# Performance work log

Hardware: AMD Instinct MI355X
Metric: run time of the kernel (lower is better)

Reference implementation:

```python
import jax, jax.numpy as jnp
import numpy as np

N = 1_000_000      # neurons (scaled-up NEURON_COUNT)
E = 20_000_000     # synapses (scaled-up NEURON_COUNT * SYNAPSE_RATIO)
IN = 4096          # input_size
OUT = 4096         # output_size
STEPS = 3


def setup_inputs() -> dict:
    key = jax.random.key(0)
    k1, k2, k3, k4, k5 = jax.random.split(key, 5)
    x = jax.random.normal(k1, (IN,), jnp.float32)
    synapse_src = jax.random.randint(k2, (E,), 0, N)
    synapse_dst = jax.random.randint(k3, (E,), 0, N)
    synapse_weights = jax.random.normal(k4, (E,), jnp.float32)
    neuron_biases = jax.random.normal(k5, (N - IN,), jnp.float32)
    input_indices = jnp.arange(IN)              # first IN neurons are inputs
    output_indices = jnp.arange(N - OUT, N)     # last OUT neurons are outputs
    non_input_indices = jnp.arange(IN, N)       # complement of input_indices
    return {
        "x": x,
        "synapse_weights": synapse_weights,
        "neuron_biases": neuron_biases,
        "synapse_src": synapse_src,
        "synapse_dst": synapse_dst,
        "input_indices": input_indices,
        "output_indices": output_indices,
        "non_input_indices": non_input_indices,
    }


def reference(x, synapse_weights, neuron_biases, synapse_src, synapse_dst,
              input_indices, output_indices, non_input_indices):
    # out_mask[i] True => neuron i is an output (skipped by tanh)
    out_mask = jnp.zeros(N, dtype=bool).at[output_indices].set(True)
    # initial state: zeros with inputs written in
    v = jnp.zeros(N, dtype=x.dtype).at[input_indices].set(x)
    for _ in range(STEPS):
        # per-edge multiply + scatter-add into destination neurons
        msgs = v[synapse_src] * synapse_weights          # [E]
        nxt = jax.ops.segment_sum(msgs, synapse_dst, num_segments=N)  # [N]
        # bias only for non-input neurons
        nxt = nxt.at[non_input_indices].add(neuron_biases)
        # tanh everywhere except output neurons
        v = jnp.where(out_mask, nxt, jnp.tanh(nxt))
    return v[output_indices]
```

## Files before the change

### kernel.cpp

```cpp
#include <hip/hip_runtime.h>

#define THREADS 256
#define BTHREADS 1024
#define SCTHREADS 1024
#define BSHIFT 11
#define BSIZE 2048
#define NBMAX 512
#define PASS_EDGES 8192
#define EPT 8
#define NPMAX 2560
typedef unsigned int u32;
typedef unsigned short u16;
typedef unsigned long long u64;


__global__ void prep_kernel(const float* __restrict__ x, const float* __restrict__ bias,
                            float* __restrict__ v, float* __restrict__ nxt,
                            int N, int IN) {
    int i = blockIdx.x * THREADS + threadIdx.x;
    if (i >= N) return;
    v[i]   = (i < IN) ? x[i] : 0.0f;
    nxt[i] = (i < IN) ? 0.0f : bias[i - IN];
}

__global__ void finalize0_kernel(float* __restrict__ v, int N, int OUT) {
    int i = blockIdx.x * THREADS + threadIdx.x;
    if (i >= N) return;
    float val = v[i];
    v[i] = (i >= N - OUT) ? val : tanhf(val);
}

__global__ void __launch_bounds__(SCTHREADS)
scatter_kernel(const int* __restrict__ src, const int* __restrict__ dst,
               const float* __restrict__ w,
               const float* __restrict__ vA,
               float* __restrict__ vB,
               uint2* __restrict__ e8, u16* __restrict__ dir,
               int E, int IN, int NB, int NP) {
    __shared__ uint2 stage[PASS_EDGES];
    __shared__ u32 hc[NBMAX];
    __shared__ u32 runStart[NBMAX + 1];

    const int tid = threadIdx.x;
    for (int i = tid; i < NBMAX; i += SCTHREADS) hc[i] = 0;
    __syncthreads();

    for (int p = blockIdx.x; p < NP; p += gridDim.x) {
        int ps = p * PASS_EDGES;
        int pe = ps + PASS_EDGES; if (pe > E) pe = E;
        int cntAll = pe - ps;

        int base = ps + tid * EPT;
        u32 pk[EPT]; u32 bk[EPT]; u32 wb[EPT];
        int cnt = 0;
        if (base + EPT <= pe) {
            int4 s0 = *(const int4*)(src + base), s1 = *(const int4*)(src + base + 4);
            int4 d0 = *(const int4*)(dst + base), d1 = *(const int4*)(dst + base + 4);
            float4 w0 = *(const float4*)(w + base), w1 = *(const float4*)(w + base + 4);
            int ss[EPT] = {s0.x, s0.y, s0.z, s0.w, s1.x, s1.y, s1.z, s1.w};
            int dd[EPT] = {d0.x, d0.y, d0.z, d0.w, d1.x, d1.y, d1.z, d1.w};
            float ww[EPT] = {w0.x, w0.y, w0.z, w0.w, w1.x, w1.y, w1.z, w1.w};
            cnt = EPT;
            #pragma unroll
            for (int i = 0; i < EPT; ++i) {
                u32 d = (u32)dd[i];
                bk[i] = d >> BSHIFT;
                pk[i] = (u32)ss[i] | ((d & (BSIZE - 1u)) << 20);
                wb[i] = __float_as_uint(ww[i]);
                if (ss[i] < IN) atomicAdd(&vB[dd[i]], vA[ss[i]] * ww[i]);
            }
        } else {
            for (int i = 0; i < EPT; ++i) {
                int e = base + i;
                if (e < pe) {
                    int s = src[e];
                    u32 d = (u32)dst[e];
                    float wv = w[e];
                    bk[cnt] = d >> BSHIFT;
                    pk[cnt] = (u32)s | ((d & (BSIZE - 1u)) << 20);
                    wb[cnt] = __float_as_uint(wv);
                    if (s < IN) atomicAdd(&vB[d], vA[s] * wv);
                    ++cnt;
                }
            }
        }

        for (int i = 0; i < cnt; ++i) atomicAdd(&hc[bk[i]], 1u);
        __syncthreads();

        if (tid < 64) {
            u32 c[8]; u32 s = 0;
            #pragma unroll
            for (int k = 0; k < 8; ++k) { c[k] = hc[tid * 8 + k]; s += c[k]; }
            u32 inc = s;
            #pragma unroll
            for (int off = 1; off < 64; off <<= 1) {
                u32 t = __shfl_up(inc, off, 64);
                if (tid >= off) inc += t;
            }
            u32 excl = inc - s;
            #pragma unroll
            for (int k = 0; k < 8; ++k) {
                runStart[tid * 8 + k] = excl;
                excl += c[k];
                hc[tid * 8 + k] = 0;
            }
            if (tid == 63) runStart[NBMAX] = excl;
        }
        __syncthreads();

        for (int i = 0; i < cnt; ++i) {
            u32 b = bk[i];
            u32 r = atomicAdd(&hc[b], 1u);
            stage[runStart[b] + r] = make_uint2(pk[i], wb[i]);
        }
        __syncthreads();

        for (int j = tid * 2; j + 1 < cntAll; j += SCTHREADS * 2)
            *(uint4*)(e8 + ps + j) = *(const uint4*)(stage + j);
        if ((cntAll & 1) && tid == 0) e8[ps + cntAll - 1] = stage[cntAll - 1];
        if (tid <= NB) dir[(u32)p * (u32)(NB + 1) + tid] = (u16)runStart[tid];
        if (tid < NBMAX) hc[tid] = 0;
        __syncthreads();
    }
}

__global__ void __launch_bounds__(BTHREADS)
bucket_step_kernel(const uint2* __restrict__ e8, const u16* __restrict__ dir,
                   const float* __restrict__ v_in, float* __restrict__ v_out,
                   const float* __restrict__ bias,
                   float* __restrict__ out,
                   int N, int IN, int OUT, int NB, int NP) {
    __shared__ float acc[BSIZE];
    __shared__ u16 rs[NPMAX], re[NPMAX];
    const int tid = threadIdx.x;
    const int b = blockIdx.x;

    for (int p = tid; p < NP; p += BTHREADS) {
        const u16* row = dir + (u32)p * (u32)(NB + 1) + b;
        rs[p] = row[0];
        re[p] = row[1];
    }
    for (int i = tid; i < BSIZE; i += BTHREADS) acc[i] = 0.0f;
    __syncthreads();

    const int sg = tid >> 4, ln = tid & 15;
    for (int p = sg; p < NP; p += BTHREADS >> 4) {
        int s0 = rs[p], s1 = re[p];
        int base = p * PASS_EDGES;
        for (int j = s0 + ln; j < s1; j += 16) {
            u64 pv = __builtin_nontemporal_load((const u64*)(e8 + base + j));
            u32 px = (u32)pv;
            float pw = __uint_as_float((u32)(pv >> 32));
            atomicAdd(&acc[px >> 20], v_in[px & 0xFFFFFu] * pw);
        }
    }
    __syncthreads();

    int nbase = b << BSHIFT;
    for (int j = tid; j < BSIZE; j += BTHREADS) {
        int idx = nbase + j;
        if (idx >= N) break;
        float val = acc[j] + (idx >= IN ? bias[idx - IN] : 0.0f);
        bool isOut = idx >= N - OUT;
        float a = isOut ? val : tanhf(val);
        v_out[idx] = a;
        if (out != nullptr && isOut) out[idx - (N - OUT)] = a;
    }
}


__global__ void edge_kernel(const int* __restrict__ src, const int* __restrict__ dst,
                            const float* __restrict__ w, const float* __restrict__ v,
                            float* __restrict__ nxt, int E) {
    int k = blockIdx.x * THREADS + threadIdx.x;
    int E4 = E >> 2;
    if (k < E4) {
        int4 s = ((const int4*)src)[k];
        int4 d = ((const int4*)dst)[k];
        float4 wv = ((const float4*)w)[k];
        atomicAdd(&nxt[d.x], v[s.x] * wv.x);
        atomicAdd(&nxt[d.y], v[s.y] * wv.y);
        atomicAdd(&nxt[d.z], v[s.z] * wv.z);
        atomicAdd(&nxt[d.w], v[s.w] * wv.w);
    }
    if (k == 0) {
        for (int e = E4 << 2; e < E; ++e)
            atomicAdd(&nxt[dst[e]], v[src[e]] * w[e]);
    }
}

__global__ void finalize_kernel(float* __restrict__ nxt, float* __restrict__ v,
                                const float* __restrict__ bias, float* __restrict__ out,
                                int N, int IN, int OUT) {
    int i = blockIdx.x * THREADS + threadIdx.x;
    if (i >= N) return;
    float val = nxt[i];
    bool isOut = (i >= N - OUT);
    float a = isOut ? val : tanhf(val);
    v[i] = a;
    nxt[i] = (i < IN) ? 0.0f : bias[i - IN];
    if (out != nullptr && isOut) out[i - (N - OUT)] = a;
}


extern "C" void kernel_launch(void* const* d_in, const int* in_sizes, int n_in,
                              void* d_out, int out_size, void* d_ws, size_t ws_size,
                              hipStream_t stream) {
    const float* x    = (const float*)d_in[0];
    const float* w    = (const float*)d_in[1];
    const float* bias = (const float*)d_in[2];
    const int* src = (const int*)d_in[3];
    const int* dst = (const int*)d_in[4];

    const int IN  = in_sizes[0];
    const int E   = in_sizes[1];
    const int N   = IN + in_sizes[2];
    const int OUT = out_size;

    const int NP = (E + PASS_EDGES - 1) / PASS_EDGES;
    const int NB = (N + BSIZE - 1) >> BSHIFT;

    uint2* e8   = (uint2*)d_ws;
    u16*   dir  = (u16*)(e8 + E);
    size_t dirB = (size_t)NP * (size_t)(NB + 1) * sizeof(u16);
    float* vA   = (float*)((char*)dir + ((dirB + 15) & ~(size_t)15));
    float* vB   = vA + N;
    size_t need = (size_t)((char*)(vB + N) - (char*)d_ws);

    int nBlocks = (N + THREADS - 1) / THREADS;

    if (ws_size >= need && N <= (NBMAX << BSHIFT) && NP <= NPMAX) {
        prep_kernel<<<nBlocks, THREADS, 0, stream>>>(x, bias, vA, vB, N, IN);
        scatter_kernel<<<512, SCTHREADS, 0, stream>>>(
            src, dst, w, vA, vB, e8, dir, E, IN, NB, NP);
        finalize0_kernel<<<nBlocks, THREADS, 0, stream>>>(vB, N, OUT);
        bucket_step_kernel<<<NB, BTHREADS, 0, stream>>>(
            e8, dir, vB, vA, bias, nullptr, N, IN, OUT, NB, NP);
        bucket_step_kernel<<<NB, BTHREADS, 0, stream>>>(
            e8, dir, vA, vB, bias, (float*)d_out, N, IN, OUT, NB, NP);
    } else {
        float* v   = (float*)d_ws;
        float* nxt = v + N;
        int eBlocks = ((E >> 2) + THREADS - 1) / THREADS;
        prep_kernel<<<nBlocks, THREADS, 0, stream>>>(x, bias, v, nxt, N, IN);
        for (int step = 0; step < 3; ++step) {
            edge_kernel<<<eBlocks, THREADS, 0, stream>>>(src, dst, w, v, nxt, E);
            float* outp = (step == 2) ? (float*)d_out : nullptr;
            finalize_kernel<<<nBlocks, THREADS, 0, stream>>>(nxt, v, bias, outp, N, IN, OUT);
        }
    }
}
```

Baseline: 668.1 us.

## Group buckets per block and split passes across blocks with global atomic merge

Each bucket-step block now covers four destination buckets, using an 8192-entry shared accumulator, and handles only a quarter of the scatter passes. Partial sums are merged into global memory with atomics, so each step now needs a memset and a separate finalize kernel for bias and tanh. Each wavefront interleaves four pass segments to keep more loads in flight. The aim is to cut the per-block cost of reading the directory, fix the load imbalance, and improve latency hiding, at the price of extra launches, global atomics and more memory traffic.

Measured after the change: 667.1 us. Within noise of the previous version (-0.1%).

```diff
diff --git a/kernel.cpp b/kernel.cpp
--- a/kernel.cpp
+++ b/kernel.cpp
@@ -8,7 +8,11 @@
 #define NBMAX 512
 #define PASS_EDGES 8192
 #define EPT 8
-#define NPMAX 2560
+#define G 4
+#define GSHIFT 2
+#define ACCSIZE 8192
+#define SPLIT 4
+#define NPSMAX 640
 typedef unsigned int u32;
 typedef unsigned short u16;
 typedef unsigned long long u64;
@@ -28,6 +32,18 @@
     if (i >= N) return;
     float val = v[i];
     v[i] = (i >= N - OUT) ? val : tanhf(val);
+}
+
+__global__ void finalize_fast_kernel(float* __restrict__ nxt, const float* __restrict__ bias,
+                                     float* __restrict__ out,
+                                     int N, int IN, int OUT) {
+    int i = blockIdx.x * THREADS + threadIdx.x;
+    if (i >= N) return;
+    float val = nxt[i] + (i >= IN ? bias[i - IN] : 0.0f);
+    bool isOut = (i >= N - OUT);
+    float a = isOut ? val : tanhf(val);
+    nxt[i] = a;
+    if (out != nullptr && isOut) out[i - (N - OUT)] = a;
 }
 
 __global__ void __launch_bounds__(SCTHREADS)
@@ -127,45 +143,74 @@
 
 __global__ void __launch_bounds__(BTHREADS)
 bucket_step_kernel(const uint2* __restrict__ e8, const u16* __restrict__ dir,
-                   const float* __restrict__ v_in, float* __restrict__ v_out,
-                   const float* __restrict__ bias,
-                   float* __restrict__ out,
-                   int N, int IN, int OUT, int NB, int NP) {
-    __shared__ float acc[BSIZE];
-    __shared__ u16 rs[NPMAX], re[NPMAX];
+                   const float* __restrict__ v_in, float* __restrict__ nxt,
+                   int N, int NB, int NP) {
+    __shared__ float acc[ACCSIZE];
+    __shared__ u16 sb[G + 1][NPSMAX];
     const int tid = threadIdx.x;
-    const int b = blockIdx.x;
-
-    for (int p = tid; p < NP; p += BTHREADS) {
-        const u16* row = dir + (u32)p * (u32)(NB + 1) + b;
-        rs[p] = row[0];
-        re[p] = row[1];
-    }
-    for (int i = tid; i < BSIZE; i += BTHREADS) acc[i] = 0.0f;
+    const int gb = blockIdx.x >> 2;
+    const int sp = blockIdx.x & 3;
+
+    const int NPS = (NP + SPLIT - 1) / SPLIT;
+    const int p0 = sp * NPS;
+    int pc = NP - p0; if (pc > NPS) pc = NPS; if (pc < 0) pc = 0;
+
+    const int b0 = gb << GSHIFT;
+    for (int idx = tid; idx < pc * (G + 1); idx += BTHREADS) {
+        int i = idx / (G + 1), k = idx - i * (G + 1);
+        int col = b0 + k; if (col > NB) col = NB;
+        sb[k][i] = dir[(u32)(p0 + i) * (u32)(NB + 1) + col];
+    }
+    for (int i = tid; i < ACCSIZE; i += BTHREADS) acc[i] = 0.0f;
     __syncthreads();
 
-    const int sg = tid >> 4, ln = tid & 15;
-    for (int p = sg; p < NP; p += BTHREADS >> 4) {
-        int s0 = rs[p], s1 = re[p];
-        int base = p * PASS_EDGES;
-        for (int j = s0 + ln; j < s1; j += 16) {
-            u64 pv = __builtin_nontemporal_load((const u64*)(e8 + base + j));
-            u32 px = (u32)pv;
-            float pw = __uint_as_float((u32)(pv >> 32));
-            atomicAdd(&acc[px >> 20], v_in[px & 0xFFFFFu] * pw);
+    const int wv = tid >> 6, ln = tid & 63;
+    for (int pp = wv; pp < pc; pp += 64) {
+        int  jj[4], je[4], eb[4];
+        u32  s1[4], s2[4], s3[4];
+        bool act[4];
+        #pragma unroll
+        for (int c = 0; c < 4; ++c) {
+            int i = pp + c * 16;
+            act[c] = false;
+            if (i < pc) {
+                u32 a0 = sb[0][i];
+                s1[c] = sb[1][i]; s2[c] = sb[2][i]; s3[c] = sb[3][i];
+                jj[c] = (int)a0 + ln;
+                je[c] = (int)sb[4][i];
+                eb[c] = (p0 + i) * PASS_EDGES;
+                act[c] = jj[c] < je[c];
+            }
+        }
+        while (act[0] | act[1] | act[2] | act[3]) {
+            u64 pv[4];
+            #pragma unroll
+            for (int c = 0; c < 4; ++c)
+                if (act[c]) pv[c] = __builtin_nontemporal_load((const u64*)(e8 + eb[c] + jj[c]));
+            float vv[4];
+            #pragma unroll
+            for (int c = 0; c < 4; ++c)
+                if (act[c]) vv[c] = v_in[(u32)pv[c] & 0xFFFFFu];
+            #pragma unroll
+            for (int c = 0; c < 4; ++c) {
+                if (act[c]) {
+                    u32 px = (u32)pv[c];
+                    u32 j  = (u32)jj[c];
+                    u32 r  = (u32)(j >= s1[c]) + (u32)(j >= s2[c]) + (u32)(j >= s3[c]);
+                    float pw = __uint_as_float((u32)(pv[c] >> 32));
+                    atomicAdd(&acc[(r << BSHIFT) + (px >> 20)], vv[c] * pw);
+                    jj[c] += 64;
+                    act[c] = jj[c] < je[c];
+                }
+            }
         }
     }
     __syncthreads();
 
-    int nbase = b << BSHIFT;
-    for (int j = tid; j < BSIZE; j += BTHREADS) {
+    int nbase = b0 << BSHIFT;
+    for (int j = tid; j < ACCSIZE; j += BTHREADS) {
         int idx = nbase + j;
-        if (idx >= N) break;
-        float val = acc[j] + (idx >= IN ? bias[idx - IN] : 0.0f);
-        bool isOut = idx >= N - OUT;
-        float a = isOut ? val : tanhf(val);
-        v_out[idx] = a;
-        if (out != nullptr && isOut) out[idx - (N - OUT)] = a;
+        if (idx < N) atomicAdd(&nxt[idx], acc[j]);
     }
 }
 
@@ -230,15 +275,20 @@
 
     int nBlocks = (N + THREADS - 1) / THREADS;
 
-    if (ws_size >= need && N <= (NBMAX << BSHIFT) && NP <= NPMAX) {
+    if (ws_size >= need && N <= (NBMAX << BSHIFT) && NP <= SPLIT * NPSMAX) {
+        const int NBG = ((NB + G - 1) >> GSHIFT);
         prep_kernel<<<nBlocks, THREADS, 0, stream>>>(x, bias, vA, vB, N, IN);
         scatter_kernel<<<512, SCTHREADS, 0, stream>>>(
             src, dst, w, vA, vB, e8, dir, E, IN, NB, NP);
         finalize0_kernel<<<nBlocks, THREADS, 0, stream>>>(vB, N, OUT);
-        bucket_step_kernel<<<NB, BTHREADS, 0, stream>>>(
-            e8, dir, vB, vA, bias, nullptr, N, IN, OUT, NB, NP);
-        bucket_step_kernel<<<NB, BTHREADS, 0, stream>>>(
-            e8, dir, vA, vB, bias, (float*)d_out, N, IN, OUT, NB, NP);
+        hipMemsetAsync(vA, 0, (size_t)N * sizeof(float), stream);
+        bucket_step_kernel<<<NBG * SPLIT, BTHREADS, 0, stream>>>(
+            e8, dir, vB, vA, N, NB, NP);
+        finalize_fast_kernel<<<nBlocks, THREADS, 0, stream>>>(vA, bias, nullptr, N, IN, OUT);
+        hipMemsetAsync(vB, 0, (size_t)N * sizeof(float), stream);
+        bucket_step_kernel<<<NBG * SPLIT, BTHREADS, 0, stream>>>(
+            e8, dir, vA, vB, N, NB, NP);
+        finalize_fast_kernel<<<nBlocks, THREADS, 0, stream>>>(vB, bias, (float*)d_out, N, IN, OUT);
     } else {
         float* v   = (float*)d_ws;
         float* nxt = v + N;
```

## Globally bucket edges by destination group and sub-sort by source tile for LDS-cached gathers

Applied to the files above, without the earlier changes.

Replaces the per-pass bucketed edge layout with a two-level global sort. A histogram and scan over 4096-neuron destination groups drives a scatter into contiguous per-group regions, and a slab sort then orders each 8192-edge slab by 8192-neuron source tile. Each consume block stages source-activation tiles in LDS, so gathers hit shared memory instead of random global reads, and flushes its accumulators with global atomics. The cost is extra preprocessing kernels, memsets, a two-way split per group with atomic merges, and a finalize kernel per step.

After: 861.6 us. 29.0% more time.

```diff
diff --git a/kernel.cpp b/kernel.cpp
--- a/kernel.cpp
+++ b/kernel.cpp
@@ -1,14 +1,16 @@
 #include <hip/hip_runtime.h>
 
 #define THREADS 256
-#define BTHREADS 1024
 #define SCTHREADS 1024
-#define BSHIFT 11
-#define BSIZE 2048
-#define NBMAX 512
 #define PASS_EDGES 8192
 #define EPT 8
-#define NPMAX 2560
+#define GSH2 12
+#define GRP2 4096
+#define NGR 256
+#define TSH 13
+#define TILE 8192
+#define NTIL 128
+#define SLAB 8192
 typedef unsigned int u32;
 typedef unsigned short u16;
 typedef unsigned long long u64;
@@ -30,25 +32,90 @@
     v[i] = (i >= N - OUT) ? val : tanhf(val);
 }
 
+__global__ void finalize_fast_kernel(float* __restrict__ nxt, const float* __restrict__ bias,
+                                     float* __restrict__ out,
+                                     int N, int IN, int OUT) {
+    int i = blockIdx.x * THREADS + threadIdx.x;
+    if (i >= N) return;
+    float val = nxt[i] + (i >= IN ? bias[i - IN] : 0.0f);
+    bool isOut = (i >= N - OUT);
+    float a = isOut ? val : tanhf(val);
+    nxt[i] = a;
+    if (out != nullptr && isOut) out[i - (N - OUT)] = a;
+}
+
+
+__global__ void histo2_kernel(const int* __restrict__ dst, u32* __restrict__ mc, int E) {
+    __shared__ u32 h[NGR];
+    for (int i = threadIdx.x; i < NGR; i += THREADS) h[i] = 0;
+    __syncthreads();
+    int stride = gridDim.x * THREADS;
+    int E4 = E >> 2;
+    for (int k = blockIdx.x * THREADS + threadIdx.x; k < E4; k += stride) {
+        int4 d = ((const int4*)dst)[k];
+        atomicAdd(&h[((u32)d.x) >> GSH2], 1u);
+        atomicAdd(&h[((u32)d.y) >> GSH2], 1u);
+        atomicAdd(&h[((u32)d.z) >> GSH2], 1u);
+        atomicAdd(&h[((u32)d.w) >> GSH2], 1u);
+    }
+    if (blockIdx.x == 0 && threadIdx.x == 0)
+        for (int e = E4 << 2; e < E; ++e) atomicAdd(&h[((u32)dst[e]) >> GSH2], 1u);
+    __syncthreads();
+    for (int i = threadIdx.x; i < NGR; i += THREADS) {
+        u32 c = h[i];
+        if (c) atomicAdd(&mc[i], c);
+    }
+}
+
+__global__ void scan2_kernel(const u32* __restrict__ mc, u32* __restrict__ mo,
+                             u32* __restrict__ gcursor, u32* __restrict__ mrow) {
+    __shared__ u32 s[NGR];
+    const int t = threadIdx.x;
+    u32 cnt = mc[t];
+    s[t] = cnt;
+    __syncthreads();
+    for (int off = 1; off < NGR; off <<= 1) {
+        u32 v = (t >= off) ? s[t - off] : 0u;
+        __syncthreads();
+        s[t] += v;
+        __syncthreads();
+    }
+    u32 excl = s[t] - cnt;
+    mo[t] = excl;
+    gcursor[t] = excl;
+    u32 rows = (cnt + SLAB - 1u) >> 13;
+    __syncthreads();
+    s[t] = rows;
+    __syncthreads();
+    for (int off = 1; off < NGR; off <<= 1) {
+        u32 v = (t >= off) ? s[t - off] : 0u;
+        __syncthreads();
+        s[t] += v;
+        __syncthreads();
+    }
+    mrow[t] = s[t] - rows;
+    if (t == NGR - 1) mrow[NGR] = s[t];
+}
+
 __global__ void __launch_bounds__(SCTHREADS)
-scatter_kernel(const int* __restrict__ src, const int* __restrict__ dst,
-               const float* __restrict__ w,
-               const float* __restrict__ vA,
-               float* __restrict__ vB,
-               uint2* __restrict__ e8, u16* __restrict__ dir,
-               int E, int IN, int NB, int NP) {
-    __shared__ uint2 stage[PASS_EDGES];
-    __shared__ u32 hc[NBMAX];
-    __shared__ u32 runStart[NBMAX + 1];
+scatter2_kernel(const int* __restrict__ src, const int* __restrict__ dst,
+                const float* __restrict__ w,
+                const float* __restrict__ vA,
+                float* __restrict__ vB,
+                u32* __restrict__ gcursor, uint2* __restrict__ e9,
+                int E, int IN, int NP) {
+    __shared__ __align__(16) uint2 stage[PASS_EDGES];
+    __shared__ u32 hc[NGR];
+    __shared__ u32 runStart[NGR + 1];
+    __shared__ u32 gpos[NGR];
 
     const int tid = threadIdx.x;
-    for (int i = tid; i < NBMAX; i += SCTHREADS) hc[i] = 0;
+    for (int i = tid; i < NGR; i += SCTHREADS) hc[i] = 0;
     __syncthreads();
 
     for (int p = blockIdx.x; p < NP; p += gridDim.x) {
         int ps = p * PASS_EDGES;
         int pe = ps + PASS_EDGES; if (pe > E) pe = E;
-        int cntAll = pe - ps;
 
         int base = ps + tid * EPT;
         u32 pk[EPT]; u32 bk[EPT]; u32 wb[EPT];
@@ -64,8 +131,8 @@
             #pragma unroll
             for (int i = 0; i < EPT; ++i) {
                 u32 d = (u32)dd[i];
-                bk[i] = d >> BSHIFT;
-                pk[i] = (u32)ss[i] | ((d & (BSIZE - 1u)) << 20);
+                bk[i] = d >> GSH2;
+                pk[i] = (u32)ss[i] | ((d & (GRP2 - 1u)) << 20);
                 wb[i] = __float_as_uint(ww[i]);
                 if (ss[i] < IN) atomicAdd(&vB[dd[i]], vA[ss[i]] * ww[i]);
             }
@@ -76,8 +143,8 @@
                     int s = src[e];
                     u32 d = (u32)dst[e];
                     float wv = w[e];
-                    bk[cnt] = d >> BSHIFT;
-                    pk[cnt] = (u32)s | ((d & (BSIZE - 1u)) << 20);
+                    bk[cnt] = d >> GSH2;
+                    pk[cnt] = (u32)s | ((d & (GRP2 - 1u)) << 20);
                     wb[cnt] = __float_as_uint(wv);
                     if (s < IN) atomicAdd(&vB[d], vA[s] * wv);
                     ++cnt;
@@ -89,26 +156,30 @@
         __syncthreads();
 
         if (tid < 64) {
-            u32 c[8]; u32 s = 0;
+            u32 c[4]; u32 ssum = 0;
             #pragma unroll
-            for (int k = 0; k < 8; ++k) { c[k] = hc[tid * 8 + k]; s += c[k]; }
-            u32 inc = s;
+            for (int k = 0; k < 4; ++k) { c[k] = hc[tid * 4 + k]; ssum += c[k]; }
+            u32 inc = ssum;
             #pragma unroll
             for (int off = 1; off < 64; off <<= 1) {
-                u32 t = __shfl_up(inc, off, 64);
-                if (tid >= off) inc += t;
-            }
-            u32 excl = inc - s;
+                u32 t2 = __shfl_up(inc, off, 64);
+                if (tid >= off) inc += t2;
+            }
+            u32 excl = inc - ssum;
             #pragma unroll
-            for (int k = 0; k < 8; ++k) {
-                runStart[tid * 8 + k] = excl;
+            for (int k = 0; k < 4; ++k) {
+                runStart[tid * 4 + k] = excl;
                 excl += c[k];
-                hc[tid * 8 + k] = 0;
-            }
-            if (tid == 63) runStart[NBMAX] = excl;
-        }
-        __syncthreads();
-
+                hc[tid * 4 + k] = 0;
+            }
+            if (tid == 63) runStart[NGR] = excl;
+        }
+        __syncthreads();
+
+        if (tid < NGR) {
+            u32 len = runStart[tid + 1] - runStart[tid];
+            gpos[tid] = len ? atomicAdd(&gcursor[tid], len) : 0u;
+        }
         for (int i = 0; i < cnt; ++i) {
             u32 b = bk[i];
             u32 r = atomicAdd(&hc[b], 1u);
@@ -116,56 +187,149 @@
         }
         __syncthreads();
 
-        for (int j = tid * 2; j + 1 < cntAll; j += SCTHREADS * 2)
-            *(uint4*)(e8 + ps + j) = *(const uint4*)(stage + j);
-        if ((cntAll & 1) && tid == 0) e8[ps + cntAll - 1] = stage[cntAll - 1];
-        if (tid <= NB) dir[(u32)p * (u32)(NB + 1) + tid] = (u16)runStart[tid];
-        if (tid < NBMAX) hc[tid] = 0;
-        __syncthreads();
-    }
-}
-
-__global__ void __launch_bounds__(BTHREADS)
-bucket_step_kernel(const uint2* __restrict__ e8, const u16* __restrict__ dir,
-                   const float* __restrict__ v_in, float* __restrict__ v_out,
-                   const float* __restrict__ bias,
-                   float* __restrict__ out,
-                   int N, int IN, int OUT, int NB, int NP) {
-    __shared__ float acc[BSIZE];
-    __shared__ u16 rs[NPMAX], re[NPMAX];
+        {
+            const int wvv = tid >> 6, lnn = tid & 63;
+            const u64* st = (const u64*)stage;
+            u64* e64 = (u64*)e9;
+            for (int b = wvv; b < NGR; b += (SCTHREADS >> 6)) {
+                u32 s0 = runStart[b], s1 = runStart[b + 1], gp = gpos[b];
+                for (u32 j = s0 + lnn; j < s1; j += 64)
+                    __builtin_nontemporal_store(st[j], e64 + gp + (j - s0));
+            }
+        }
+        if (tid < NGR) hc[tid] = 0;
+        __syncthreads();
+    }
+}
+
+__global__ void __launch_bounds__(1024)
+slabsort_kernel(uint2* __restrict__ e9, const u32* __restrict__ mo,
+                const u32* __restrict__ mc, const u32* __restrict__ mrow,
+                u16* __restrict__ dir2) {
+    __shared__ __align__(16) uint2 stg[SLAB];
+    __shared__ u32 hist[NTIL];
+    __shared__ u32 rs2[NTIL + 1];
+    __shared__ int sg;
+
     const int tid = threadIdx.x;
-    const int b = blockIdx.x;
-
-    for (int p = tid; p < NP; p += BTHREADS) {
-        const u16* row = dir + (u32)p * (u32)(NB + 1) + b;
-        rs[p] = row[0];
-        re[p] = row[1];
-    }
-    for (int i = tid; i < BSIZE; i += BTHREADS) acc[i] = 0.0f;
-    __syncthreads();
-
-    const int sg = tid >> 4, ln = tid & 15;
-    for (int p = sg; p < NP; p += BTHREADS >> 4) {
-        int s0 = rs[p], s1 = re[p];
-        int base = p * PASS_EDGES;
-        for (int j = s0 + ln; j < s1; j += 16) {
-            u64 pv = __builtin_nontemporal_load((const u64*)(e8 + base + j));
-            u32 px = (u32)pv;
-            float pw = __uint_as_float((u32)(pv >> 32));
-            atomicAdd(&acc[px >> 20], v_in[px & 0xFFFFFu] * pw);
-        }
-    }
-    __syncthreads();
-
-    int nbase = b << BSHIFT;
-    for (int j = tid; j < BSIZE; j += BTHREADS) {
-        int idx = nbase + j;
-        if (idx >= N) break;
-        float val = acc[j] + (idx >= IN ? bias[idx - IN] : 0.0f);
-        bool isOut = idx >= N - OUT;
-        float a = isOut ? val : tanhf(val);
-        v_out[idx] = a;
-        if (out != nullptr && isOut) out[idx - (N - OUT)] = a;
+    const u32 row = blockIdx.x;
+    if (row >= mrow[NGR]) return;
+
+    if (tid == 0) {
+        int lo = 0, hi = NGR;
+        while (hi - lo > 1) {
+            int mid = (lo + hi) >> 1;
+            if (mrow[mid] <= row) lo = mid; else hi = mid;
+        }
+        sg = lo;
+    }
+    if (tid < NTIL) hist[tid] = 0;
+    __syncthreads();
+
+    const int g = sg;
+    const u32 q = row - mrow[g];
+    const u32 a = mo[g] + (q << 13);
+    u32 m = mc[g] - (q << 13); if (m > SLAB) m = SLAB;
+
+    u32 kr[8], wr2[8];
+    #pragma unroll
+    for (int i = 0; i < 8; ++i) {
+        u32 j = (u32)tid + (u32)i * 1024u;
+        if (j < m) {
+            u64 rv = __builtin_nontemporal_load((const u64*)e9 + a + j);
+            kr[i] = (u32)rv; wr2[i] = (u32)(rv >> 32);
+            atomicAdd(&hist[(kr[i] >> TSH) & (NTIL - 1u)], 1u);
+        }
+    }
+    __syncthreads();
+
+    if (tid < 64) {
+        u32 c0 = hist[tid * 2], c1 = hist[tid * 2 + 1];
+        u32 s = c0 + c1, inc = s;
+        #pragma unroll
+        for (int off = 1; off < 64; off <<= 1) {
+            u32 t2 = __shfl_up(inc, off, 64);
+            if (tid >= off) inc += t2;
+        }
+        u32 excl = inc - s;
+        rs2[tid * 2] = excl;
+        rs2[tid * 2 + 1] = excl + c0;
+        hist[tid * 2] = 0; hist[tid * 2 + 1] = 0;
+        if (tid == 63) rs2[NTIL] = inc;
+    }
+    __syncthreads();
+
+    #pragma unroll
+    for (int i = 0; i < 8; ++i) {
+        u32 j = (u32)tid + (u32)i * 1024u;
+        if (j < m) {
+            u32 key = kr[i];
+            u32 tl = (key >> TSH) & (NTIL - 1u);
+            u32 rk = atomicAdd(&hist[tl], 1u);
+            u32 nk = (key & 0x1FFFu) | ((key >> 20) << TSH);
+            stg[rs2[tl] + rk] = make_uint2(nk, wr2[i]);
+        }
+    }
+    __syncthreads();
+
+    {
+        const u64* st = (const u64*)stg;
+        u64* out = (u64*)e9 + a;
+        for (u32 j = tid; j < m; j += 1024)
+            __builtin_nontemporal_store(st[j], out + j);
+    }
+    if (tid <= NTIL)
+        dir2[row * (u32)(NTIL + 1) + (u32)tid] = (u16)rs2[tid];
+}
+
+__global__ void __launch_bounds__(1024)
+consume2_kernel(const uint2* __restrict__ e9, const u16* __restrict__ dir2,
+                const u32* __restrict__ mo, const u32* __restrict__ mc,
+                const u32* __restrict__ mrow,
+                const float* __restrict__ v_in, float* __restrict__ nxt, int N) {
+    __shared__ float acc[GRP2];
+    __shared__ float vt[TILE];
+    const int tid = threadIdx.x, wv = tid >> 6, ln = tid & 63;
+    const int g = blockIdx.x >> 1, h = blockIdx.x & 1;
+
+    const u32 cnt  = mc[g];
+    const u32 rowb = mrow[g];
+    const u32 nq   = (cnt + SLAB - 1u) >> 13;
+    const u32 eb0  = mo[g];
+
+    for (int i = tid; i < GRP2; i += 1024) acc[i] = 0.0f;
+
+    for (int s = h * (NTIL / 2); s < (h + 1) * (NTIL / 2); ++s) {
+        int vb = s << TSH;
+        if (vb >= N) break;
+        if (vb + TILE <= N) {
+            for (int j = tid; j < TILE / 4; j += 1024)
+                *(float4*)&vt[j * 4] = *(const float4*)(v_in + vb + j * 4);
+        } else {
+            for (int j = tid; j < TILE; j += 1024) {
+                int idx = vb + j;
+                vt[j] = (idx < N) ? v_in[idx] : 0.0f;
+            }
+        }
+        __syncthreads();
+        for (u32 q = wv; q < nq; q += 16) {
+            const u16* r2 = dir2 + (rowb + q) * (u32)(NTIL + 1) + (u32)s;
+            u32 a2 = r2[0], b2 = r2[1];
+            const u64* basee = (const u64*)e9 + eb0 + (q << 13);
+            for (u32 j = a2 + ln; j < b2; j += 64) {
+                u64 pv = __builtin_nontemporal_load(basee + j);
+                u32 k = (u32)pv;
+                float pw = __uint_as_float((u32)(pv >> 32));
+                atomicAdd(&acc[k >> TSH], vt[k & (TILE - 1u)] * pw);
+            }
+        }
+        __syncthreads();
+    }
+
+    const int nb = g << GSH2;
+    for (int j = tid; j < GRP2; j += 1024) {
+        int idx = nb + j;
+        if (idx < N) atomicAdd(&nxt[idx], acc[j]);
     }
 }
 
@@ -219,26 +383,39 @@
     const int OUT = out_size;
 
     const int NP = (E + PASS_EDGES - 1) / PASS_EDGES;
-    const int NB = (N + BSIZE - 1) >> BSHIFT;
-
-    uint2* e8   = (uint2*)d_ws;
-    u16*   dir  = (u16*)(e8 + E);
-    size_t dirB = (size_t)NP * (size_t)(NB + 1) * sizeof(u16);
-    float* vA   = (float*)((char*)dir + ((dirB + 15) & ~(size_t)15));
+    const int NG = (N + GRP2 - 1) >> GSH2;
+    const int NROWS = NP + NG + 4;
+
+    int nBlocks = (N + THREADS - 1) / THREADS;
+
+    uint2* e9   = (uint2*)d_ws;
+    size_t off  = (size_t)E * 8;
+    u16*   dir2 = (u16*)((char*)d_ws + off);
+    off += ((size_t)NROWS * (NTIL + 1) * 2 + 15) & ~(size_t)15;
+    u32*   mc   = (u32*)((char*)d_ws + off);
+    u32*   mo   = mc + NGR;
+    u32*   gcur = mo + NGR;
+    u32*   mrow = gcur + NGR;
+    off += ((size_t)(NGR * 3 + NGR + 1) * 4 + 15) & ~(size_t)15;
+    float* vA   = (float*)((char*)d_ws + off);
     float* vB   = vA + N;
-    size_t need = (size_t)((char*)(vB + N) - (char*)d_ws);
-
-    int nBlocks = (N + THREADS - 1) / THREADS;
-
-    if (ws_size >= need && N <= (NBMAX << BSHIFT) && NP <= NPMAX) {
+    size_t need = off + (size_t)N * 8;
+
+    if (ws_size >= need && N <= (NGR << GSH2)) {
+        hipMemsetAsync(mc, 0, NGR * sizeof(u32), stream);
         prep_kernel<<<nBlocks, THREADS, 0, stream>>>(x, bias, vA, vB, N, IN);
-        scatter_kernel<<<512, SCTHREADS, 0, stream>>>(
-            src, dst, w, vA, vB, e8, dir, E, IN, NB, NP);
+        histo2_kernel<<<1024, THREADS, 0, stream>>>(dst, mc, E);
+        scan2_kernel<<<1, NGR, 0, stream>>>(mc, mo, gcur, mrow);
+        scatter2_kernel<<<512, SCTHREADS, 0, stream>>>(
+            src, dst, w, vA, vB, gcur, e9, E, IN, NP);
         finalize0_kernel<<<nBlocks, THREADS, 0, stream>>>(vB, N, OUT);
-        bucket_step_kernel<<<NB, BTHREADS, 0, stream>>>(
-            e8, dir, vB, vA, bias, nullptr, N, IN, OUT, NB, NP);
-        bucket_step_kernel<<<NB, BTHREADS, 0, stream>>>(
-            e8, dir, vA, vB, bias, (float*)d_out, N, IN, OUT, NB, NP);
+        slabsort_kernel<<<NROWS, 1024, 0, stream>>>(e9, mo, mc, mrow, dir2);
+        hipMemsetAsync(vA, 0, (size_t)N * sizeof(float), stream);
+        consume2_kernel<<<NG * 2, 1024, 0, stream>>>(e9, dir2, mo, mc, mrow, vB, vA, N);
+        finalize_fast_kernel<<<nBlocks, THREADS, 0, stream>>>(vA, bias, nullptr, N, IN, OUT);
+        hipMemsetAsync(vB, 0, (size_t)N * sizeof(float), stream);
+        consume2_kernel<<<NG * 2, 1024, 0, stream>>>(e9, dir2, mo, mc, mrow, vA, vB, N);
+        finalize_fast_kernel<<<nBlocks, THREADS, 0, stream>>>(vB, bias, (float*)d_out, N, IN, OUT);
     } else {
         float* v   = (float*)d_ws;
         float* nxt = v + N;
```
